# Optimization experiments

Measured on AMD Instinct MI355X. Metric: run time of the kernel, lower is better.

Reference implementation:

```python
import jax, jax.numpy as jnp
import numpy as np

R = 12            # search_radius
P = 2 * R + 1     # 25x25 search window
DIV = 512.0       # self.div_num; T = DIV**-0.5


def _relu_l2norm(x, axis=1, eps=1e-12):
    # matches F.relu followed by F.normalize(p=2, dim=1)
    x = jax.nn.relu(x)
    n = jnp.sqrt(jnp.sum(x * x, axis=axis, keepdims=True))
    return x / jnp.maximum(n, eps)


def setup_inputs() -> dict:
    key = jax.random.key(0)
    k1, k2 = jax.random.split(key)
    feat1_video = jax.random.normal(k1, (8, 512, 4, 30, 30), dtype=jnp.float32)  # r50_feat1 (pre relu/norm)
    feat2_img = jax.random.normal(k2, (8, 512, 30, 30), dtype=jnp.float32)       # img_feat2 (pre relu/norm)
    return {"feat1_video": feat1_video, "feat2_img": feat2_img}


def reference(feat1_video, feat2_img):
    # relu + channel L2-normalize, as in forward() before compute_corr_softmax
    video = _relu_l2norm(feat1_video)          # [B,C,T,H,W]  -> r50_feat2 arg
    patch = _relu_l2norm(feat2_img)            # [B,C,H,W]    -> patch_feat1 arg
    B, C, T, H, W = video.shape

    vpad = jnp.pad(video, ((0, 0), (0, 0), (0, 0), (R, R), (R, R)))

    # all 625 (dh, dw) window offsets, vmapped into one fused correlation
    offsets = jnp.stack(
        jnp.meshgrid(jnp.arange(P), jnp.arange(P), indexing="ij"), axis=-1
    ).reshape(-1, 2)  # [P*P, 2]

    def shift_corr(off):
        win = jax.lax.dynamic_slice(
            vpad, (0, 0, 0, off[0], off[1]), (B, C, T, H, W)
        )
        return jnp.einsum("bcthw,bchw->bthw", win, patch)

    corr = jax.vmap(shift_corr)(offsets)               # [P*P, B, T, H, W]
    corr = jnp.transpose(corr, (1, 2, 0, 3, 4))        # [B, T, P*P, H, W]

    # torch: div by div_num**-0.5, then softmax(corr / T) with T = div_num**-0.5
    Tparam = DIV ** (-0.5)
    corr = corr / (DIV ** (-0.5)) / Tparam             # == corr * 512
    sm = jax.nn.softmax(corr, axis=2)

    # validity mask: output pixel y with shift h=dh-R is valid iff 0 <= y+h < H
    dh = jnp.arange(P)
    ys = jnp.arange(H)
    xs = jnp.arange(W)
    valid_h = ((ys[None, :] + dh[:, None] - R) >= 0) & ((ys[None, :] + dh[:, None] - R) < H)  # [P,H]
    valid_w = ((xs[None, :] + dh[:, None] - R) >= 0) & ((xs[None, :] + dh[:, None] - R) < W)  # [P,W]
    valid = valid_h[:, None, :, None] & valid_w[None, :, None, :]  # [P,P,H,W]
    valid = valid.reshape(P * P, H, W)

    out = jnp.where(valid[None, None], sm, jnp.float32(-1.0))      # [B,T,P*P,H,W]
    return out.reshape(B, T, P, P, H, W)
```

## Files before the change

### kernel.cpp

```cpp
#include <hip/hip_runtime.h>

#define RR 12
#define PD 25
#define PP 625
#define HH 30
#define WW 30
#define HWD 900
#define CD 512
#define BD 8
#define TD 4
#define CSTRIDE 628
#define ROWPKB 32768

typedef __attribute__((ext_vector_type(4))) int i32x4;
typedef __attribute__((ext_vector_type(16))) int i32x16;

__global__ __launch_bounds__(256) void norm_pack_kernel(const float* __restrict__ in,
                                                        unsigned char* __restrict__ outp,
                                                        int c_stride, int t_count) {
    int row = blockIdx.x;
    int plane = blockIdx.y;
    int b = plane / t_count;
    int t = plane - b * t_count;
    size_t base = (size_t)b * CD * c_stride + (size_t)t * HWD + row * WW;
    __shared__ float tile[30][516];
    __shared__ float inv[30];
    int tid = threadIdx.x;
    for (int it = 0; it < 64; ++it) {
        int lin = it * 256 + tid;
        int c = lin >> 5, p = lin & 31;
        if (p < 30) tile[p][c] = fmaxf(in[base + (size_t)c * c_stride + p], 0.f);
    }
    __syncthreads();
    if ((tid >> 3) < 30) {
        int p = tid >> 3, s8 = tid & 7;
        float acc = 0.f;
#pragma unroll
        for (int j = 0; j < 16; ++j) {
            const float4 v = *reinterpret_cast<const float4*>(&tile[p][(s8 + j * 8) * 4]);
            acc += v.x * v.x + v.y * v.y + v.z * v.z + v.w * v.w;
        }
        acc += __shfl_xor(acc, 1);
        acc += __shfl_xor(acc, 2);
        acc += __shfl_xor(acc, 4);
        if (s8 == 0) inv[p] = 1.0f / fmaxf(sqrtf(acc), 1e-12f);
    }
    __syncthreads();
    unsigned char* ob = outp + (size_t)(plane * 30 + row) * ROWPKB;
    for (int sl = tid; sl < 1024; sl += 256) {
        int ks = sl >> 6, ln = sl & 63;
        int x = ln & 31;
        if (x > 29) x = 29;
        int kb = ks * 32 + (ln >> 5) * 16;
        float iv = inv[x];
        union { signed char c[16]; i32x4 v; } p1, p2;
#pragma unroll
        for (int j = 0; j < 16; ++j) {
            float nv = tile[x][kb + j] * iv;
            float s1 = rintf(nv * 127.f);
            float r = nv * 127.f - s1;
            float s2 = rintf(r * 254.f);
            p1.c[j] = (signed char)(int)s1;
            p2.c[j] = (signed char)(int)s2;
        }
        *(i32x4*)(ob + (size_t)ks * 2048 + ln * 16) = p1.v;
        *(i32x4*)(ob + (size_t)ks * 2048 + 1024 + ln * 16) = p2.v;
    }
}

__global__ __launch_bounds__(1024, 4) void corr_kernel(
    const unsigned char* __restrict__ Apk, const unsigned char* __restrict__ Bpk,
    float* __restrict__ out) {
    int gid = blockIdx.x;
    int r = gid & 7;
    int x_ = gid >> 3;
    int btl = x_ / 30;
    int h = x_ - btl * 30;
    int bt = r * 4 + btl;
    int b = r;

    __shared__ float corr[HH * CSTRIDE];
    __shared__ unsigned char alds[ROWPKB];
    __shared__ float is_lds[HH];
    int tid = threadIdx.x;
    int wid = tid >> 6, lane = tid & 63;

    for (int i = tid; i < HH * CSTRIDE; i += 1024) corr[i] = 0.f;
    {
        const uint4* src = (const uint4*)(Apk + (size_t)(b * 30 + h) * ROWPKB);
        uint4* dst = (uint4*)alds;
#pragma unroll
        for (int i = 0; i < 2; ++i) dst[i * 1024 + tid] = src[i * 1024 + tid];
    }
    const unsigned char* bplane = Bpk + (size_t)bt * 30 * ROWPKB + lane * 16;
    int dh_lo = max(0, RR - h);
    int dh_hi = min(PD - 1, HH - 1 + RR - h);
    __syncthreads();

    const unsigned char* albase = alds + lane * 16;
    for (int dh = dh_lo + wid; dh <= dh_hi; dh += 16) {
        int y = h + dh - RR;
        const unsigned char* bbase = bplane + (size_t)y * ROWPKB;
        i32x16 s11, s12, s21, s22;
#pragma unroll
        for (int i = 0; i < 16; ++i) { s11[i] = 0; s12[i] = 0; s21[i] = 0; s22[i] = 0; }
#pragma unroll 8
        for (int ks = 0; ks < 16; ++ks) {
            i32x4 a1 = *(const i32x4*)(albase + ks * 2048);
            i32x4 a2 = *(const i32x4*)(albase + ks * 2048 + 1024);
            i32x4 b1 = *(const i32x4*)(bbase + ks * 2048);
            i32x4 b2 = *(const i32x4*)(bbase + ks * 2048 + 1024);
            s11 = __builtin_amdgcn_mfma_i32_32x32x32_i8(a1, b1, s11, 0, 0, 0);
            s12 = __builtin_amdgcn_mfma_i32_32x32x32_i8(a1, b2, s12, 0, 0, 0);
            s21 = __builtin_amdgcn_mfma_i32_32x32x32_i8(a2, b1, s21, 0, 0, 0);
            s22 = __builtin_amdgcn_mfma_i32_32x32x32_i8(a2, b2, s22, 0, 0, 0);
        }
        int x = lane & 31;
        if (x < 30) {
            int rbase = 4 * (lane >> 5);
#pragma unroll
            for (int rr = 0; rr < 16; ++rr) {
                int w = (rr & 3) + 8 * (rr >> 2) + rbase;
                int dw = x - w + RR;
                if (w < 30 && (unsigned)dw < (unsigned)PD) {
                    float c = ((float)s11[rr] +
                               (float)(s12[rr] + s21[rr]) * (1.0f / 254.0f) +
                               (float)s22[rr] * (1.0f / 64516.0f)) * (1.0f / 16129.0f);
                    corr[w * CSTRIDE + dh * PD + dw] = c;
                }
            }
        }
    }
    __syncthreads();

    for (int w = wid; w < WW; w += 16) {
        float m = 0.f;
        for (int i = lane; i < PP; i += 64) m = fmaxf(m, corr[w * CSTRIDE + i]);
        m = fmaxf(m, __shfl_xor(m, 1));
        m = fmaxf(m, __shfl_xor(m, 2));
        m = fmaxf(m, __shfl_xor(m, 4));
        m = fmaxf(m, __shfl_xor(m, 8));
        m = fmaxf(m, __shfl_xor(m, 16));
        m = fmaxf(m, __shfl_xor(m, 32));
        float s = 0.f;
        for (int i = lane; i < PP; i += 64) {
            float e = __expf(512.f * (corr[w * CSTRIDE + i] - m));
            s += e;
            corr[w * CSTRIDE + i] = e;
        }
        s += __shfl_xor(s, 1);
        s += __shfl_xor(s, 2);
        s += __shfl_xor(s, 4);
        s += __shfl_xor(s, 8);
        s += __shfl_xor(s, 16);
        s += __shfl_xor(s, 32);
        if (lane == 0) is_lds[w] = 1.0f / s;
    }
    __syncthreads();

    float* obase = out + (size_t)bt * PP * HWD + h * WW;
    for (int idx = tid; idx < PP * WW; idx += 1024) {
        int i = idx / 30;
        int w = idx - i * 30;
        int dh = i / 25, dw = i - dh * 25;
        bool valid = ((unsigned)(h + dh - RR) < (unsigned)HH) &&
                     ((unsigned)(w + dw - RR) < (unsigned)WW);
        float val = -1.0f;
        if (valid) val = corr[w * CSTRIDE + i] * is_lds[w];
        obase[(size_t)i * HWD + w] = val;
    }
}

extern "C" void kernel_launch(void* const* d_in, const int* in_sizes, int n_in,
                              void* d_out, int out_size, void* d_ws, size_t ws_size,
                              hipStream_t stream) {
    const float* feat1 = (const float*)d_in[0];
    const float* feat2 = (const float*)d_in[1];
    float* out = (float*)d_out;
    unsigned char* Apk = (unsigned char*)d_ws;
    unsigned char* Bpk = Apk + (size_t)BD * 30 * ROWPKB;

    norm_pack_kernel<<<dim3(30, 8), 256, 0, stream>>>(feat2, Apk, HWD, 1);
    norm_pack_kernel<<<dim3(30, 32), 256, 0, stream>>>(feat1, Bpk, TD * HWD, TD);
    corr_kernel<<<dim3(960), 1024, 0, stream>>>(Apk, Bpk, out);
}
```

Baseline: 119.8 us.

## Merge norm-pack launches, shrink corr blocks to 512 threads, read A from global

Combines the two normalize/pack launches into a single grid that branches on plane index, removing one kernel launch. The correlation kernel drops from 1024 to 512 threads, removes the 32KB LDS staging of the A row and reads A fragments directly from global/L2, which cuts LDS use so more blocks can be resident per CU. The dequant scale is folded into the softmax exponent constant, and the output loop uses a power-of-two index split instead of division by 30. The trade-off is redundant global reads of A per wave and fewer waves per block for the MFMA loop.

```diff
diff --git a/kernel.cpp b/kernel.cpp
--- a/kernel.cpp
+++ b/kernel.cpp
@@ -11,18 +11,33 @@
 #define TD 4
 #define CSTRIDE 628
 #define ROWPKB 32768
+#define QSCALE 16129.0f
+#define EXPK (512.0f / QSCALE)
 
 typedef __attribute__((ext_vector_type(4))) int i32x4;
 typedef __attribute__((ext_vector_type(16))) int i32x16;
 
-__global__ __launch_bounds__(256) void norm_pack_kernel(const float* __restrict__ in,
-                                                        unsigned char* __restrict__ outp,
-                                                        int c_stride, int t_count) {
+__global__ __launch_bounds__(256) void norm_pack_kernel(const float* __restrict__ inP,
+                                                        const float* __restrict__ inV,
+                                                        unsigned char* __restrict__ outA,
+                                                        unsigned char* __restrict__ outB) {
     int row = blockIdx.x;
     int plane = blockIdx.y;
-    int b = plane / t_count;
-    int t = plane - b * t_count;
-    size_t base = (size_t)b * CD * c_stride + (size_t)t * HWD + row * WW;
+    const float* in;
+    size_t base;
+    int c_stride;
+    unsigned char* ob;
+    if (plane < 8) {
+        in = inP; c_stride = HWD;
+        base = (size_t)plane * CD * HWD + row * WW;
+        ob = outA + (size_t)(plane * 30 + row) * ROWPKB;
+    } else {
+        int bt = plane - 8;
+        int b = bt >> 2, t = bt & 3;
+        in = inV; c_stride = TD * HWD;
+        base = (size_t)b * CD * (TD * HWD) + (size_t)t * HWD + row * WW;
+        ob = outB + (size_t)(bt * 30 + row) * ROWPKB;
+    }
     __shared__ float tile[30][516];
     __shared__ float inv[30];
     int tid = threadIdx.x;
@@ -46,7 +61,6 @@
         if (s8 == 0) inv[p] = 1.0f / fmaxf(sqrtf(acc), 1e-12f);
     }
     __syncthreads();
-    unsigned char* ob = outp + (size_t)(plane * 30 + row) * ROWPKB;
     for (int sl = tid; sl < 1024; sl += 256) {
         int ks = sl >> 6, ln = sl & 63;
         int x = ln & 31;
@@ -68,7 +82,7 @@
     }
 }
 
-__global__ __launch_bounds__(1024, 4) void corr_kernel(
+__global__ __launch_bounds__(512, 4) void corr_kernel(
     const unsigned char* __restrict__ Apk, const unsigned char* __restrict__ Bpk,
     float* __restrict__ out) {
     int gid = blockIdx.x;
@@ -80,25 +94,19 @@
     int b = r;
 
     __shared__ float corr[HH * CSTRIDE];
-    __shared__ unsigned char alds[ROWPKB];
     __shared__ float is_lds[HH];
     int tid = threadIdx.x;
     int wid = tid >> 6, lane = tid & 63;
 
-    for (int i = tid; i < HH * CSTRIDE; i += 1024) corr[i] = 0.f;
-    {
-        const uint4* src = (const uint4*)(Apk + (size_t)(b * 30 + h) * ROWPKB);
-        uint4* dst = (uint4*)alds;
-#pragma unroll
-        for (int i = 0; i < 2; ++i) dst[i * 1024 + tid] = src[i * 1024 + tid];
-    }
+    for (int i = tid; i < HH * CSTRIDE; i += 512) corr[i] = 0.f;
+
+    const unsigned char* abase = Apk + (size_t)(b * 30 + h) * ROWPKB + lane * 16;
     const unsigned char* bplane = Bpk + (size_t)bt * 30 * ROWPKB + lane * 16;
     int dh_lo = max(0, RR - h);
     int dh_hi = min(PD - 1, HH - 1 + RR - h);
     __syncthreads();
 
-    const unsigned char* albase = alds + lane * 16;
-    for (int dh = dh_lo + wid; dh <= dh_hi; dh += 16) {
+    for (int dh = dh_lo + wid; dh <= dh_hi; dh += 8) {
         int y = h + dh - RR;
         const unsigned char* bbase = bplane + (size_t)y * ROWPKB;
         i32x16 s11, s12, s21, s22;
@@ -106,8 +114,8 @@
         for (int i = 0; i < 16; ++i) { s11[i] = 0; s12[i] = 0; s21[i] = 0; s22[i] = 0; }
 #pragma unroll 8
         for (int ks = 0; ks < 16; ++ks) {
-            i32x4 a1 = *(const i32x4*)(albase + ks * 2048);
-            i32x4 a2 = *(const i32x4*)(albase + ks * 2048 + 1024);
+            i32x4 a1 = *(const i32x4*)(abase + ks * 2048);
+            i32x4 a2 = *(const i32x4*)(abase + ks * 2048 + 1024);
             i32x4 b1 = *(const i32x4*)(bbase + ks * 2048);
             i32x4 b2 = *(const i32x4*)(bbase + ks * 2048 + 1024);
             s11 = __builtin_amdgcn_mfma_i32_32x32x32_i8(a1, b1, s11, 0, 0, 0);
@@ -123,9 +131,9 @@
                 int w = (rr & 3) + 8 * (rr >> 2) + rbase;
                 int dw = x - w + RR;
                 if (w < 30 && (unsigned)dw < (unsigned)PD) {
-                    float c = ((float)s11[rr] +
-                               (float)(s12[rr] + s21[rr]) * (1.0f / 254.0f) +
-                               (float)s22[rr] * (1.0f / 64516.0f)) * (1.0f / 16129.0f);
+                    float c = fmaf((float)(s12[rr] + s21[rr]), 1.0f / 254.0f,
+                                   (float)s11[rr]) +
+                              (float)s22[rr] * (1.0f / 64516.0f);
                     corr[w * CSTRIDE + dh * PD + dw] = c;
                 }
             }
@@ -133,7 +141,7 @@
     }
     __syncthreads();
 
-    for (int w = wid; w < WW; w += 16) {
+    for (int w = wid; w < WW; w += 8) {
         float m = 0.f;
         for (int i = lane; i < PP; i += 64) m = fmaxf(m, corr[w * CSTRIDE + i]);
         m = fmaxf(m, __shfl_xor(m, 1));
@@ -144,7 +152,7 @@
         m = fmaxf(m, __shfl_xor(m, 32));
         float s = 0.f;
         for (int i = lane; i < PP; i += 64) {
-            float e = __expf(512.f * (corr[w * CSTRIDE + i] - m));
+            float e = __expf(EXPK * (corr[w * CSTRIDE + i] - m));
             s += e;
             corr[w * CSTRIDE + i] = e;
         }
@@ -159,15 +167,17 @@
     __syncthreads();
 
     float* obase = out + (size_t)bt * PP * HWD + h * WW;
-    for (int idx = tid; idx < PP * WW; idx += 1024) {
-        int i = idx / 30;
-        int w = idx - i * 30;
-        int dh = i / 25, dw = i - dh * 25;
-        bool valid = ((unsigned)(h + dh - RR) < (unsigned)HH) &&
-                     ((unsigned)(w + dw - RR) < (unsigned)WW);
-        float val = -1.0f;
-        if (valid) val = corr[w * CSTRIDE + i] * is_lds[w];
-        obase[(size_t)i * HWD + w] = val;
+    for (int idx = tid; idx < PP * 32; idx += 512) {
+        int w = idx & 31;
+        if (w < 30) {
+            int i = idx >> 5;
+            int dh = i / 25, dw = i - dh * 25;
+            bool valid = ((unsigned)(h + dh - RR) < (unsigned)HH) &&
+                         ((unsigned)(w + dw - RR) < (unsigned)WW);
+            float val = -1.0f;
+            if (valid) val = corr[w * CSTRIDE + i] * is_lds[w];
+            obase[(size_t)i * HWD + w] = val;
+        }
     }
 }
 
@@ -180,7 +190,6 @@
     unsigned char* Apk = (unsigned char*)d_ws;
     unsigned char* Bpk = Apk + (size_t)BD * 30 * ROWPKB;
 
-    norm_pack_kernel<<<dim3(30, 8), 256, 0, stream>>>(feat2, Apk, HWD, 1);
-    norm_pack_kernel<<<dim3(30, 32), 256, 0, stream>>>(feat1, Bpk, TD * HWD, TD);
-    corr_kernel<<<dim3(960), 1024, 0, stream>>>(Apk, Bpk, out);
+    norm_pack_kernel<<<dim3(30, 40), 256, 0, stream>>>(feat2, feat1, Apk, Bpk);
+    corr_kernel<<<dim3(960), 512, 0, stream>>>(Apk, Bpk, out);
 }
```

New measurement: 126.3 us. 5.4% more time.
